# Kernel optimization log

Hardware: AMD Instinct MI355X
Metric: run time of the kernel (lower is better)

The kernel has to match this reference:

```python
import jax, jax.numpy as jnp
import numpy as np

N_NODES = 30000
N_EDGES = 480000
IN_CH = 64
CHANNELS = [64, 64, 64]
N_HEADS = 4
BN_EPS = 1e-5


def setup_inputs() -> dict:
    key = jax.random.key(0)
    ks = jax.random.split(key, 32)
    x = jax.random.normal(ks[0], (N_NODES, IN_CH), dtype=jnp.float32)
    # edges with no self loops (module removes then re-adds self loops)
    src = jax.random.randint(ks[1], (N_EDGES,), 0, N_NODES)
    off = jax.random.randint(ks[2], (N_EDGES,), 1, N_NODES)
    dst = (src + off) % N_NODES
    edge_index = jnp.stack([src, dst]).astype(jnp.int64)

    inp = {"x": x, "edge_index": edge_index}
    in_ch = IN_CH
    ki = 3
    for li, out_ch in enumerate(CHANNELS):
        # torch init: uniform_ for linear/u weights, N(0, 0.1) for c and bias
        inp[f"W{li}"] = jax.random.uniform(ks[ki], (out_ch * N_HEADS, in_ch), dtype=jnp.float32)
        inp[f"U{li}"] = jax.random.uniform(ks[ki + 1], (N_HEADS, in_ch), dtype=jnp.float32)
        inp[f"c{li}"] = 0.1 * jax.random.normal(ks[ki + 2], (N_HEADS,), dtype=jnp.float32)
        inp[f"b{li}"] = 0.1 * jax.random.normal(ks[ki + 3], (out_ch,), dtype=jnp.float32)
        if li < len(CHANNELS) - 1:  # BN only between layers
            inp[f"g{li}"] = jnp.ones((out_ch,), dtype=jnp.float32)
            inp[f"bt{li}"] = jnp.zeros((out_ch,), dtype=jnp.float32)
        ki += 4
        in_ch = out_ch
    return inp


def _feast_conv(x, src, dst, W, U, c, b, n_nodes):
    """FeatureSteeredConvolution with mean aggregation (trans-invariant attention)."""
    xi = x[dst]  # central nodes  [E, in]
    xj = x[src]  # neighbors      [E, in]
    logits = (xi - xj) @ U.T + c            # [E, M]
    attn = jax.nn.softmax(logits, axis=1)   # [E, M]
    e = src.shape[0]
    out_ch = W.shape[0] // N_HEADS
    xjw = (xj @ W.T).reshape(e, N_HEADS, out_ch)       # [E, M, out]
    msg = jnp.einsum('em,emo->eo', attn, xjw)           # [E, out]
    agg = jax.ops.segment_sum(msg, dst, num_segments=n_nodes)
    cnt = jax.ops.segment_sum(jnp.ones((e,), msg.dtype), dst, num_segments=n_nodes)
    return agg / cnt[:, None] + b  # self loops guarantee cnt >= 1


def _batch_norm(x, gamma, beta):
    # BatchNorm1d, training mode: biased batch statistics
    mu = x.mean(axis=0)
    var = x.var(axis=0)
    return (x - mu) * jax.lax.rsqrt(var + BN_EPS) * gamma + beta


def reference(x, edge_index, W0, U0, c0, b0, g0, bt0, W1, U1, c1, b1, g1, bt1, W2, U2, c2, b2):
    n = x.shape[0]
    loops = jnp.arange(n, dtype=edge_index.dtype)
    src = jnp.concatenate([edge_index[0], loops])
    dst = jnp.concatenate([edge_index[1], loops])
    h = _feast_conv(x, src, dst, W0, U0, c0, b0, n)
    h = _batch_norm(jax.nn.relu(h), g0, bt0)
    h = _feast_conv(h, src, dst, W1, U1, c1, b1, n)
    h = _batch_norm(jax.nn.relu(h), g1, bt1)
    return _feast_conv(h, src, dst, W2, U2, c2, b2, n)
```

## Files before the change

### kernel.cpp

```cpp
#include <hip/hip_runtime.h>

#define NN 30000
#define NE 480000
#define BN_EPS 1e-5f
#define EBLK 1875
#define FBLK 3750
#define PKBLK 469
#define NSHARD 16

typedef __attribute__((ext_vector_type(8))) short bf16x8;
typedef __attribute__((ext_vector_type(4))) float f32x4;

__device__ __forceinline__ unsigned short f2bf(float x) {
    unsigned int u = __float_as_uint(x);
    return (unsigned short)((u + 0x7fffu + ((u >> 16) & 1u)) >> 16);
}
__device__ __forceinline__ float bf2f(unsigned short h) {
    return __uint_as_float(((unsigned int)h) << 16);
}

__device__ __forceinline__ int detect64(const unsigned int* __restrict__ ei) {
    unsigned int v = ei[1] | ei[3] | ei[5] | ei[7] |
                     ei[9] | ei[11] | ei[13] | ei[15];
    return v == 0u;
}
__device__ __forceinline__ int load_idx(const void* ei, int is64, int pos) {
    if (is64) return (int)((const long long*)ei)[pos];
    return ((const int*)ei)[pos];
}

__global__ __launch_bounds__(256) void k_prep_hist(const float* __restrict__ x,
                                                   const float* __restrict__ W0,
                                                   const float* __restrict__ W1,
                                                   const float* __restrict__ W2,
                                                   const void* __restrict__ ei,
                                                   ushort* __restrict__ xbf,
                                                   ushort* __restrict__ wb,
                                                   int4* __restrict__ statz,
                                                   int* __restrict__ degi) {
    int b = blockIdx.x;
    int tid = threadIdx.x;
    if (b < 1875) {
        int t = b * 256 + tid;
        float4 v = reinterpret_cast<const float4*>(x)[t];
        ushort4 o;
        o.x = f2bf(v.x); o.y = f2bf(v.y); o.z = f2bf(v.z); o.w = f2bf(v.w);
        reinterpret_cast<ushort4*>(xbf)[t] = o;
    } else if (b < 2067) {
        int t2 = (b - 1875) * 256 + tid;
        int layer = t2 >> 14;
        int r = t2 & 16383;
        int ot = r >> 12;
        int kb = (r >> 9) & 7;
        int l = (r >> 3) & 63;
        int e = r & 7;
        int k = kb * 32 + (l >> 4) * 8 + e;
        int o = ot * 16 + (l & 15);
        int m = k >> 6;
        int kk = k & 63;
        const float* W = (layer == 0) ? W0 : (layer == 1) ? W1 : W2;
        wb[t2] = f2bf(W[(m * 64 + o) * 64 + kk]);
    } else if (b < 2071) {
        statz[(b - 2067) * 256 + tid] = make_int4(0, 0, 0, 0);
    } else {
        int e = (b - 2071) * 256 + tid;
        int is64 = detect64((const unsigned int*)ei);
        int d = load_idx(ei, is64, NE + e);
        atomicAdd(&degi[d], 1);
    }
}

__global__ __launch_bounds__(1024) void k_scan(const int* __restrict__ degi,
                                               int* __restrict__ rowptr) {
    __shared__ int buf[30720];
    __shared__ int sm[1024];
    int t = threadIdx.x;
    for (int i = t; i < 30720; i += 1024)
        buf[i] = (i < NN) ? degi[i] : 0;
    __syncthreads();
    const int PER = 30;
    int base = t * PER;
    int loc[PER];
    int sum = 0;
#pragma unroll
    for (int i = 0; i < PER; ++i) {
        loc[i] = sum;
        sum += buf[base + i];
    }
    sm[t] = sum;
    __syncthreads();
    for (int off = 1; off < 1024; off <<= 1) {
        int add = (t >= off) ? sm[t - off] : 0;
        __syncthreads();
        sm[t] += add;
        __syncthreads();
    }
    int tb = sm[t] - sum;
#pragma unroll
    for (int i = 0; i < PER; ++i) {
        int idx = base + i;
        if (idx < NN) rowptr[idx] = tb + loc[i];
    }
    if (t == 0) rowptr[NN] = NE;
}

__device__ __forceinline__ void dev_pk0(const float* __restrict__ h,
                                        const float* __restrict__ U,
                                        float* __restrict__ pout, int vb) {
    __shared__ float usc_s[4][64];
    int t = threadIdx.x;
    {
        int m = t >> 6, k = t & 63;
        usc_s[m][k] = U[m * 64 + k];
    }
    __syncthreads();
    int idx = vb * 256 + t;
    if (idx < NN * 4) {
        int n = idx >> 2, m = idx & 3;
        const float4* hn = reinterpret_cast<const float4*>(h) + (size_t)n * 16;
        const float* um = usc_s[m];
        float a = 0.0f;
#pragma unroll
        for (int j = 0; j < 16; ++j) {
            float4 hv = hn[j];
            a += hv.x * um[4 * j + 0] + hv.y * um[4 * j + 1] +
                 hv.z * um[4 * j + 2] + hv.w * um[4 * j + 3];
        }
        pout[idx] = a;
    }
}

__global__ __launch_bounds__(256) void k_scatter_pk0(const void* __restrict__ ei,
                                                     const int* __restrict__ rowptr,
                                                     int* __restrict__ degi,
                                                     int* __restrict__ csr,
                                                     const float* __restrict__ x,
                                                     const float* __restrict__ U0,
                                                     float* __restrict__ p) {
    if (blockIdx.x < EBLK) {
        int is64 = detect64((const unsigned int*)ei);
        int e = blockIdx.x * 256 + threadIdx.x;
        int s = load_idx(ei, is64, e);
        int d = load_idx(ei, is64, NE + e);
        int old = atomicSub(&degi[d], 1);
        csr[rowptr[d] + old - 1] = s;
    } else {
        dev_pk0(x, U0, p, blockIdx.x - EBLK);
    }
}

__global__ __launch_bounds__(256) void k_pk(const ushort* __restrict__ hbf,
                                            const float* __restrict__ U,
                                            const float* __restrict__ statsS,
                                            const float* __restrict__ g,
                                            const float* __restrict__ W,
                                            const float* __restrict__ bt,
                                            float* __restrict__ pout,
                                            float* __restrict__ cstv_out,
                                            float* __restrict__ scv_out) {
    __shared__ float usc_s[4][64];
    __shared__ float sc_l[64];
    __shared__ float sh_l[64];
    int t = threadIdx.x;
    if (t < 64) {
        float s1 = 0.0f, s2 = 0.0f;
#pragma unroll
        for (int sh = 0; sh < NSHARD; ++sh) {
            s1 += statsS[sh * 128 + t];
            s2 += statsS[sh * 128 + 64 + t];
        }
        const float invN = 1.0f / (float)NN;
        float mu = s1 * invN;
        float var = s2 * invN - mu * mu;
        float sc = rsqrtf(var + BN_EPS) * g[t];
        sc_l[t] = sc;
        sh_l[t] = bt[t] - mu * sc;
        if (blockIdx.x == 0) scv_out[t] = sc;
    }
    __syncthreads();
    {
        int m = t >> 6, k = t & 63;
        usc_s[m][k] = U[m * 64 + k] * sc_l[k];
    }
    __syncthreads();
    int idx = blockIdx.x * 256 + t;
    if (idx < NN * 4) {
        int n = idx >> 2, m = idx & 3;
        const uint4* hn = reinterpret_cast<const uint4*>(hbf + (size_t)n * 64);
        const float* um = usc_s[m];
        float a = 0.0f;
#pragma unroll
        for (int j = 0; j < 8; ++j) {
            uint4 v = hn[j];
            a += bf2f((unsigned short)v.x) * um[8 * j + 0] +
                 bf2f((unsigned short)(v.x >> 16)) * um[8 * j + 1] +
                 bf2f((unsigned short)v.y) * um[8 * j + 2] +
                 bf2f((unsigned short)(v.y >> 16)) * um[8 * j + 3] +
                 bf2f((unsigned short)v.z) * um[8 * j + 4] +
                 bf2f((unsigned short)(v.z >> 16)) * um[8 * j + 5] +
                 bf2f((unsigned short)v.w) * um[8 * j + 6] +
                 bf2f((unsigned short)(v.w >> 16)) * um[8 * j + 7];
        }
        pout[idx] = a;
    }
    if (blockIdx.x == 0) {
        float s = 0.0f;
        const float* wr = W + (size_t)t * 64;
#pragma unroll 8
        for (int k = 0; k < 64; ++k) s += sh_l[k] * wr[k];
        cstv_out[t] = s;
    }
}

template <int FOLD, int STATS>
__global__ __launch_bounds__(512, 4) void k_fused(const int* __restrict__ rowptr,
                                                  const int* __restrict__ csr,
                                                  const float* __restrict__ p,
                                                  const ushort* __restrict__ hbf_in,
                                                  const float* __restrict__ cvec,
                                                  const float* __restrict__ scv,
                                                  const float* __restrict__ cstvg,
                                                  const ushort* __restrict__ wb,
                                                  const float* __restrict__ bvec,
                                                  float* __restrict__ hout,
                                                  ushort* __restrict__ hbfout,
                                                  float* __restrict__ stats_out) {
    __shared__ float4 attn_s[8][64];
    __shared__ int src_s[8][64];
    __shared__ ushort zrow[8][272];
    __shared__ float4 zs_s[8];
    __shared__ float cstv_s[256];

    int t = threadIdx.x;
    int wid = t >> 6;
    int lane = t & 63;
    int n = blockIdx.x * 8 + wid;
    const float4* p4 = reinterpret_cast<const float4*>(p);

    if (FOLD && t < 256) cstv_s[t] = cstvg[t];

    float scl = FOLD ? scv[lane] : 1.0f;

    float4 cv = make_float4(cvec[0], cvec[1], cvec[2], cvec[3]);
    float smx = fmaxf(fmaxf(cv.x, cv.y), fmaxf(cv.z, cv.w));
    float se0 = __expf(cv.x - smx), se1 = __expf(cv.y - smx);
    float se2 = __expf(cv.z - smx), se3 = __expf(cv.w - smx);
    float sinv = 1.0f / (se0 + se1 + se2 + se3);
    float sl0 = se0 * sinv, sl1 = se1 * sinv, sl2 = se2 * sinv, sl3 = se3 * sinv;

    float4 pd = p4[n];
    float4 pdc = make_float4(pd.x + cv.x, pd.y + cv.y, pd.z + cv.z, pd.w + cv.w);
    float hs = bf2f(hbf_in[(unsigned)(n * 64 + lane)]);
    float acc0 = sl0 * hs, acc1 = sl1 * hs, acc2 = sl2 * hs, acc3 = sl3 * hs;
    float zt0 = sl0, zt1 = sl1, zt2 = sl2, zt3 = sl3;

    int start = rowptr[n];
    int end = rowptr[n + 1];
    for (int j = start; j < end; j += 64) {
        int chunk = end - j;
        if (chunk > 64) chunk = 64;
        if (lane < chunk) {
            int s = csr[j + lane];
            float4 q = p4[(unsigned)s];
            float l0 = pdc.x - q.x;
            float l1 = pdc.y - q.y;
            float l2 = pdc.z - q.z;
            float l3 = pdc.w - q.w;
            float mx = fmaxf(fmaxf(l0, l1), fmaxf(l2, l3));
            float e0 = __expf(l0 - mx);
            float e1 = __expf(l1 - mx);
            float e2 = __expf(l2 - mx);
            float e3 = __expf(l3 - mx);
            float inv = 1.0f / (e0 + e1 + e2 + e3);
            attn_s[wid][lane] = make_float4(e0 * inv, e1 * inv, e2 * inv, e3 * inv);
            src_s[wid][lane] = s;
        }
        int k = 0;
        for (; k + 4 <= chunk; k += 4) {
            float4 a0 = attn_s[wid][k];
            int s0 = src_s[wid][k];
            float4 a1 = attn_s[wid][k + 1];
            int s1 = src_s[wid][k + 1];
            float4 a2 = attn_s[wid][k + 2];
            int s2 = src_s[wid][k + 2];
            float4 a3 = attn_s[wid][k + 3];
            int s3 = src_s[wid][k + 3];
            float h0 = bf2f(hbf_in[(unsigned)(s0 * 64 + lane)]);
            float h1 = bf2f(hbf_in[(unsigned)(s1 * 64 + lane)]);
            float h2 = bf2f(hbf_in[(unsigned)(s2 * 64 + lane)]);
            float h3 = bf2f(hbf_in[(unsigned)(s3 * 64 + lane)]);
            acc0 += a0.x * h0 + a1.x * h1 + a2.x * h2 + a3.x * h3;
            acc1 += a0.y * h0 + a1.y * h1 + a2.y * h2 + a3.y * h3;
            acc2 += a0.z * h0 + a1.z * h1 + a2.z * h2 + a3.z * h3;
            acc3 += a0.w * h0 + a1.w * h1 + a2.w * h2 + a3.w * h3;
            zt0 += a0.x + a1.x + a2.x + a3.x;
            zt1 += a0.y + a1.y + a2.y + a3.y;
            zt2 += a0.z + a1.z + a2.z + a3.z;
            zt3 += a0.w + a1.w + a2.w + a3.w;
        }
        for (; k < chunk; ++k) {
            float4 a0 = attn_s[wid][k];
            int s0 = src_s[wid][k];
            float h0 = bf2f(hbf_in[(unsigned)(s0 * 64 + lane)]);
            acc0 += a0.x * h0;
            acc1 += a0.y * h0;
            acc2 += a0.z * h0;
            acc3 += a0.w * h0;
            zt0 += a0.x; zt1 += a0.y; zt2 += a0.z; zt3 += a0.w;
        }
    }

    float invD = 1.0f / (float)(end - start + 1);
    float s = invD * scl;
    {
        ushort* zr = &zrow[wid][0];
        zr[lane]       = f2bf(acc0 * s);
        zr[64 + lane]  = f2bf(acc1 * s);
        zr[128 + lane] = f2bf(acc2 * s);
        zr[192 + lane] = f2bf(acc3 * s);
        if (lane == 0)
            zs_s[wid] = make_float4(zt0 * invD, zt1 * invD, zt2 * invD, zt3 * invD);
    }
    __syncthreads();

    if (wid >= 4) return;

    int col = lane & 15;
    int grp = lane >> 4;
    int r = (col < 8) ? col : 7;
    const ushort* zr = &zrow[r][0];
    const ushort* wbp = wb + ((size_t)(wid * 8) * 64 + lane) * 8;
    f32x4 acc = {0.0f, 0.0f, 0.0f, 0.0f};
#pragma unroll
    for (int kb = 0; kb < 8; ++kb) {
        bf16x8 a = *reinterpret_cast<const bf16x8*>(zr + kb * 32 + grp * 8);
        bf16x8 b = *reinterpret_cast<const bf16x8*>(wbp + (size_t)kb * 512);
        acc = __builtin_amdgcn_mfma_f32_16x16x32_bf16(a, b, acc, 0, 0, 0);
    }

    float ls = 0.0f, lq = 0.0f;
    if (grp < 2) {
        int n0 = blockIdx.x * 8;
        int o = wid * 16 + col;
        float bval = bvec[o];
#pragma unroll
        for (int i = 0; i < 4; ++i) {
            int nn = n0 + grp * 4 + i;
            float v = acc[i] + bval;
            if (FOLD) {
                float4 zv = zs_s[grp * 4 + i];
                v += zv.x * cstv_s[o] + zv.y * cstv_s[64 + o] +
                     zv.z * cstv_s[128 + o] + zv.w * cstv_s[192 + o];
            }
            if (STATS) {
                v = fmaxf(v, 0.0f);
                hbfout[(size_t)nn * 64 + o] = f2bf(v);
                ls += v;
                lq += v * v;
            } else {
                hout[(size_t)nn * 64 + o] = v;
            }
        }
        if (STATS) {
            ls += __shfl_xor(ls, 16, 64);
            lq += __shfl_xor(lq, 16, 64);
            if (lane < 16) {
                float* so = stats_out + (blockIdx.x & (NSHARD - 1)) * 128;
                atomicAdd(&so[o], ls);
                atomicAdd(&so[64 + o], lq);
            }
        }
    }
}

extern "C" void kernel_launch(void* const* d_in, const int* in_sizes, int n_in,
                              void* d_out, int out_size, void* d_ws, size_t ws_size,
                              hipStream_t stream) {
    const float* x = (const float*)d_in[0];
    const void* ei = d_in[1];
    const float* W0 = (const float*)d_in[2];
    const float* U0 = (const float*)d_in[3];
    const float* c0 = (const float*)d_in[4];
    const float* b0 = (const float*)d_in[5];
    const float* g0 = (const float*)d_in[6];
    const float* bt0 = (const float*)d_in[7];
    const float* W1 = (const float*)d_in[8];
    const float* U1 = (const float*)d_in[9];
    const float* c1 = (const float*)d_in[10];
    const float* b1 = (const float*)d_in[11];
    const float* g1 = (const float*)d_in[12];
    const float* bt1 = (const float*)d_in[13];
    const float* W2 = (const float*)d_in[14];
    const float* U2 = (const float*)d_in[15];
    const float* c2 = (const float*)d_in[16];
    const float* b2 = (const float*)d_in[17];

    ushort* xbf = (ushort*)d_ws;
    ushort* hbfA = xbf + (size_t)NN * 64;
    ushort* hbfB = hbfA + (size_t)NN * 64;
    float* p = (float*)(hbfB + (size_t)NN * 64);
    float* cstv = p + (size_t)NN * 4;
    float* scv = cstv + 256;
    int* degi = (int*)(scv + 64);
    float* statsA = (float*)(degi + NN);
    int* rowptr = (int*)(statsA + 4096);
    int* csr = rowptr + NN + 4;
    ushort* wb = (ushort*)(csr + NE);
    float* stats0 = statsA;
    float* stats1 = statsA + 2048;

    hipMemsetAsync(degi, 0, sizeof(int) * NN, stream);
    k_prep_hist<<<3946, 256, 0, stream>>>(x, W0, W1, W2, ei, xbf, wb,
                                          (int4*)statsA, degi);
    k_scan<<<1, 1024, 0, stream>>>(degi, rowptr);
    k_scatter_pk0<<<EBLK + PKBLK, 256, 0, stream>>>(ei, rowptr, degi, csr,
                                                    x, U0, p);

    k_fused<0, 1><<<FBLK, 512, 0, stream>>>(rowptr, csr, p, xbf, c0,
                                            nullptr, nullptr, wb, b0,
                                            nullptr, hbfA, stats0);
    k_pk<<<PKBLK, 256, 0, stream>>>(hbfA, U1, stats0, g0, W1, bt0, p, cstv, scv);
    k_fused<1, 1><<<FBLK, 512, 0, stream>>>(rowptr, csr, p, hbfA, c1,
                                            scv, cstv, wb + 16384, b1,
                                            nullptr, hbfB, stats1);
    k_pk<<<PKBLK, 256, 0, stream>>>(hbfB, U2, stats1, g1, W2, bt1, p, cstv, scv);
    k_fused<1, 0><<<FBLK, 512, 0, stream>>>(rowptr, csr, p, hbfB, c2,
                                            scv, cstv, wb + 32768, b2,
                                            (float*)d_out, nullptr, nullptr);
}
```

Measured before the change: 259.2 us.

## Sort nodes by in-degree bucket to balance warps in fused conv kernels

```diff
diff --git a/kernel.cpp b/kernel.cpp
--- a/kernel.cpp
+++ b/kernel.cpp
@@ -4,6 +4,7 @@
 #define NE 480000
 #define BN_EPS 1e-5f
 #define EBLK 1875
+#define PERMBLK 118
 #define FBLK 3750
 #define PKBLK 469
 #define NSHARD 16
@@ -60,10 +61,11 @@
         int kk = k & 63;
         const float* W = (layer == 0) ? W0 : (layer == 1) ? W1 : W2;
         wb[t2] = f2bf(W[(m * 64 + o) * 64 + kk]);
-    } else if (b < 2071) {
-        statz[(b - 2067) * 256 + tid] = make_int4(0, 0, 0, 0);
+    } else if (b < 2072) {
+        int i = (b - 2067) * 256 + tid;
+        if (i < 1040) statz[i] = make_int4(0, 0, 0, 0);
     } else {
-        int e = (b - 2071) * 256 + tid;
+        int e = (b - 2072) * 256 + tid;
         int is64 = detect64((const unsigned int*)ei);
         int d = load_idx(ei, is64, NE + e);
         atomicAdd(&degi[d], 1);
@@ -71,21 +73,30 @@
 }
 
 __global__ __launch_bounds__(1024) void k_scan(const int* __restrict__ degi,
-                                               int* __restrict__ rowptr) {
+                                               int* __restrict__ rowptr,
+                                               int* __restrict__ dbase) {
     __shared__ int buf[30720];
     __shared__ int sm[1024];
+    __shared__ int whist[16][64];
     int t = threadIdx.x;
     for (int i = t; i < 30720; i += 1024)
         buf[i] = (i < NN) ? degi[i] : 0;
+    whist[t >> 6][t & 63] = 0;
     __syncthreads();
     const int PER = 30;
     int base = t * PER;
+    int wv = t >> 6;
     int loc[PER];
     int sum = 0;
 #pragma unroll
     for (int i = 0; i < PER; ++i) {
+        int d = buf[base + i];
         loc[i] = sum;
-        sum += buf[base + i];
+        sum += d;
+        if (base + i < NN) {
+            int bn = d > 63 ? 63 : d;
+            atomicAdd(&whist[wv][bn], 1);
+        }
     }
     sm[t] = sum;
     __syncthreads();
@@ -102,6 +113,22 @@
         if (idx < NN) rowptr[idx] = tb + loc[i];
     }
     if (t == 0) rowptr[NN] = NE;
+    __syncthreads();
+    if (t < 64) {
+        int s = 0;
+#pragma unroll
+        for (int w = 0; w < 16; ++w) s += whist[w][t];
+        sm[t] = s;
+    }
+    __syncthreads();
+    if (t == 0) {
+        int run = 0;
+        for (int bn = 0; bn < 64; ++bn) {
+            int v = sm[bn];
+            dbase[bn] = run;
+            run += v;
+        }
+    }
 }
 
 __device__ __forceinline__ void dev_pk0(const float* __restrict__ h,
@@ -134,6 +161,9 @@
                                                      const int* __restrict__ rowptr,
                                                      int* __restrict__ degi,
                                                      int* __restrict__ csr,
+                                                     const int* __restrict__ dbase,
+                                                     int* __restrict__ dcur,
+                                                     int* __restrict__ nperm,
                                                      const float* __restrict__ x,
                                                      const float* __restrict__ U0,
                                                      float* __restrict__ p) {
@@ -144,8 +174,16 @@
         int d = load_idx(ei, is64, NE + e);
         int old = atomicSub(&degi[d], 1);
         csr[rowptr[d] + old - 1] = s;
+    } else if (blockIdx.x < EBLK + PERMBLK) {
+        int idx = (blockIdx.x - EBLK) * 256 + threadIdx.x;
+        if (idx < NN) {
+            int deg = rowptr[idx + 1] - rowptr[idx];
+            int bn = deg > 63 ? 63 : deg;
+            int pos = dbase[bn] + atomicAdd(&dcur[bn], 1);
+            nperm[pos] = idx;
+        }
     } else {
-        dev_pk0(x, U0, p, blockIdx.x - EBLK);
+        dev_pk0(x, U0, p, blockIdx.x - EBLK - PERMBLK);
     }
 }
 
@@ -213,7 +251,8 @@
 }
 
 template <int FOLD, int STATS>
-__global__ __launch_bounds__(512, 4) void k_fused(const int* __restrict__ rowptr,
+__global__ __launch_bounds__(512, 4) void k_fused(const int* __restrict__ nperm,
+                                                  const int* __restrict__ rowptr,
                                                   const int* __restrict__ csr,
                                                   const float* __restrict__ p,
                                                   const ushort* __restrict__ hbf_in,
@@ -229,12 +268,14 @@
     __shared__ int src_s[8][64];
     __shared__ ushort zrow[8][272];
     __shared__ float4 zs_s[8];
+    __shared__ int nid_s[8];
     __shared__ float cstv_s[256];
 
     int t = threadIdx.x;
     int wid = t >> 6;
     int lane = t & 63;
-    int n = blockIdx.x * 8 + wid;
+    int n = nperm[blockIdx.x * 8 + wid];
+    if (lane == 0) nid_s[wid] = n;
     const float4* p4 = reinterpret_cast<const float4*>(p);
 
     if (FOLD && t < 256) cstv_s[t] = cstvg[t];
@@ -340,12 +381,11 @@
 
     float ls = 0.0f, lq = 0.0f;
     if (grp < 2) {
-        int n0 = blockIdx.x * 8;
         int o = wid * 16 + col;
         float bval = bvec[o];
 #pragma unroll
         for (int i = 0; i < 4; ++i) {
-            int nn = n0 + grp * 4 + i;
+            int nn = nid_s[grp * 4 + i];
             float v = acc[i] + bval;
             if (FOLD) {
                 float4 zv = zs_s[grp * 4 + i];
@@ -403,28 +443,31 @@
     float* scv = cstv + 256;
     int* degi = (int*)(scv + 64);
     float* statsA = (float*)(degi + NN);
-    int* rowptr = (int*)(statsA + 4096);
+    int* dcur = (int*)(statsA + 4096);
+    int* dbase = dcur + 64;
+    int* rowptr = dbase + 64;
     int* csr = rowptr + NN + 4;
     ushort* wb = (ushort*)(csr + NE);
+    int* nperm = (int*)(wb + 3 * 16384);
     float* stats0 = statsA;
     float* stats1 = statsA + 2048;
 
     hipMemsetAsync(degi, 0, sizeof(int) * NN, stream);
-    k_prep_hist<<<3946, 256, 0, stream>>>(x, W0, W1, W2, ei, xbf, wb,
+    k_prep_hist<<<3947, 256, 0, stream>>>(x, W0, W1, W2, ei, xbf, wb,
                                           (int4*)statsA, degi);
-    k_scan<<<1, 1024, 0, stream>>>(degi, rowptr);
-    k_scatter_pk0<<<EBLK + PKBLK, 256, 0, stream>>>(ei, rowptr, degi, csr,
-                                                    x, U0, p);
-
-    k_fused<0, 1><<<FBLK, 512, 0, stream>>>(rowptr, csr, p, xbf, c0,
+    k_scan<<<1, 1024, 0, stream>>>(degi, rowptr, dbase);
+    k_scatter_pk0<<<EBLK + PERMBLK + PKBLK, 256, 0, stream>>>(
+        ei, rowptr, degi, csr, dbase, dcur, nperm, x, U0, p);
+
+    k_fused<0, 1><<<FBLK, 512, 0, stream>>>(nperm, rowptr, csr, p, xbf, c0,
                                             nullptr, nullptr, wb, b0,
                                             nullptr, hbfA, stats0);
     k_pk<<<PKBLK, 256, 0, stream>>>(hbfA, U1, stats0, g0, W1, bt0, p, cstv, scv);
-    k_fused<1, 1><<<FBLK, 512, 0, stream>>>(rowptr, csr, p, hbfA, c1,
+    k_fused<1, 1><<<FBLK, 512, 0, stream>>>(nperm, rowptr, csr, p, hbfA, c1,
                                             scv, cstv, wb + 16384, b1,
                                             nullptr, hbfB, stats1);
     k_pk<<<PKBLK, 256, 0, stream>>>(hbfB, U2, stats1, g1, W2, bt1, p, cstv, scv);
-    k_fused<1, 0><<<FBLK, 512, 0, stream>>>(rowptr, csr, p, hbfB, c2,
+    k_fused<1, 0><<<FBLK, 512, 0, stream>>>(nperm, rowptr, csr, p, hbfB, c2,
                                             scv, cstv, wb + 32768, b2,
                                             (float*)d_out, nullptr, nullptr);
 }
```

Result: slower. 324.3 us (+25.1%).

## Compute edge attention block-wide over all 8 nodes' edges in one pass

Applied to the files above, without the earlier changes.

```diff
diff --git a/kernel.cpp b/kernel.cpp
--- a/kernel.cpp
+++ b/kernel.cpp
@@ -225,8 +225,10 @@
                                                   float* __restrict__ hout,
                                                   ushort* __restrict__ hbfout,
                                                   float* __restrict__ stats_out) {
-    __shared__ float4 attn_s[8][64];
-    __shared__ int src_s[8][64];
+    __shared__ int r_s[9];
+    __shared__ float4 pdc_s[8];
+    __shared__ float4 attn_f[512];
+    __shared__ int src_f[512];
     __shared__ ushort zrow[8][272];
     __shared__ float4 zs_s[8];
     __shared__ float cstv_s[256];
@@ -234,34 +236,48 @@
     int t = threadIdx.x;
     int wid = t >> 6;
     int lane = t & 63;
-    int n = blockIdx.x * 8 + wid;
+    int n0 = blockIdx.x * 8;
+    int n = n0 + wid;
     const float4* p4 = reinterpret_cast<const float4*>(p);
 
     if (FOLD && t < 256) cstv_s[t] = cstvg[t];
 
+    float4 cv = make_float4(cvec[0], cvec[1], cvec[2], cvec[3]);
+    if (t < 9) r_s[t] = rowptr[n0 + t];
+    if (t >= 16 && t < 24) {
+        int i = t - 16;
+        float4 pd = p4[n0 + i];
+        pdc_s[i] = make_float4(pd.x + cv.x, pd.y + cv.y, pd.z + cv.z, pd.w + cv.w);
+    }
+
     float scl = FOLD ? scv[lane] : 1.0f;
 
-    float4 cv = make_float4(cvec[0], cvec[1], cvec[2], cvec[3]);
     float smx = fmaxf(fmaxf(cv.x, cv.y), fmaxf(cv.z, cv.w));
     float se0 = __expf(cv.x - smx), se1 = __expf(cv.y - smx);
     float se2 = __expf(cv.z - smx), se3 = __expf(cv.w - smx);
     float sinv = 1.0f / (se0 + se1 + se2 + se3);
     float sl0 = se0 * sinv, sl1 = se1 * sinv, sl2 = se2 * sinv, sl3 = se3 * sinv;
 
-    float4 pd = p4[n];
-    float4 pdc = make_float4(pd.x + cv.x, pd.y + cv.y, pd.z + cv.z, pd.w + cv.w);
     float hs = bf2f(hbf_in[(unsigned)(n * 64 + lane)]);
     float acc0 = sl0 * hs, acc1 = sl1 * hs, acc2 = sl2 * hs, acc3 = sl3 * hs;
     float zt0 = sl0, zt1 = sl1, zt2 = sl2, zt3 = sl3;
 
-    int start = rowptr[n];
-    int end = rowptr[n + 1];
-    for (int j = start; j < end; j += 64) {
-        int chunk = end - j;
-        if (chunk > 64) chunk = 64;
-        if (lane < chunk) {
-            int s = csr[j + lane];
+    __syncthreads();
+    int base = r_s[0];
+    int endb = r_s[8];
+    int Eb = endb - base;
+    int gs = r_s[wid];
+    int ge = r_s[wid + 1];
+
+    for (int eb = 0; eb < Eb; eb += 512) {
+        int j = base + eb + t;
+        if (j < endb) {
+            int i = 0;
+#pragma unroll
+            for (int qq = 1; qq < 8; ++qq) i += (j >= r_s[qq]);
+            int s = csr[j];
             float4 q = p4[(unsigned)s];
+            float4 pdc = pdc_s[i];
             float l0 = pdc.x - q.x;
             float l1 = pdc.y - q.y;
             float l2 = pdc.z - q.z;
@@ -272,19 +288,25 @@
             float e2 = __expf(l2 - mx);
             float e3 = __expf(l3 - mx);
             float inv = 1.0f / (e0 + e1 + e2 + e3);
-            attn_s[wid][lane] = make_float4(e0 * inv, e1 * inv, e2 * inv, e3 * inv);
-            src_s[wid][lane] = s;
-        }
+            attn_f[t] = make_float4(e0 * inv, e1 * inv, e2 * inv, e3 * inv);
+            src_f[t] = s;
+        }
+        __syncthreads();
+
+        int from = gs > base + eb ? gs : base + eb;
+        int to = ge < base + eb + 512 ? ge : base + eb + 512;
+        int li = from - base - eb;
+        int cnt = to - from;
         int k = 0;
-        for (; k + 4 <= chunk; k += 4) {
-            float4 a0 = attn_s[wid][k];
-            int s0 = src_s[wid][k];
-            float4 a1 = attn_s[wid][k + 1];
-            int s1 = src_s[wid][k + 1];
-            float4 a2 = attn_s[wid][k + 2];
-            int s2 = src_s[wid][k + 2];
-            float4 a3 = attn_s[wid][k + 3];
-            int s3 = src_s[wid][k + 3];
+        for (; k + 4 <= cnt; k += 4) {
+            float4 a0 = attn_f[li + k];
+            int s0 = src_f[li + k];
+            float4 a1 = attn_f[li + k + 1];
+            int s1 = src_f[li + k + 1];
+            float4 a2 = attn_f[li + k + 2];
+            int s2 = src_f[li + k + 2];
+            float4 a3 = attn_f[li + k + 3];
+            int s3 = src_f[li + k + 3];
             float h0 = bf2f(hbf_in[(unsigned)(s0 * 64 + lane)]);
             float h1 = bf2f(hbf_in[(unsigned)(s1 * 64 + lane)]);
             float h2 = bf2f(hbf_in[(unsigned)(s2 * 64 + lane)]);
@@ -298,9 +320,9 @@
             zt2 += a0.z + a1.z + a2.z + a3.z;
             zt3 += a0.w + a1.w + a2.w + a3.w;
         }
-        for (; k < chunk; ++k) {
-            float4 a0 = attn_s[wid][k];
-            int s0 = src_s[wid][k];
+        for (; k < cnt; ++k) {
+            float4 a0 = attn_f[li + k];
+            int s0 = src_f[li + k];
             float h0 = bf2f(hbf_in[(unsigned)(s0 * 64 + lane)]);
             acc0 += a0.x * h0;
             acc1 += a0.y * h0;
@@ -308,9 +330,10 @@
             acc3 += a0.w * h0;
             zt0 += a0.x; zt1 += a0.y; zt2 += a0.z; zt3 += a0.w;
         }
-    }
-
-    float invD = 1.0f / (float)(end - start + 1);
+        __syncthreads();
+    }
+
+    float invD = 1.0f / (float)(ge - gs + 1);
     float s = invD * scl;
     {
         ushort* zr = &zrow[wid][0];
@@ -340,7 +363,6 @@
 
     float ls = 0.0f, lq = 0.0f;
     if (grp < 2) {
-        int n0 = blockIdx.x * 8;
         int o = wid * 16 + col;
         float bval = bvec[o];
 #pragma unroll
```

Result: slower. 265.2 us (+2.3%).
